# Kernel optimization log

Measured on AMD Instinct MI355X. Metric: run time of the kernel, lower is better.

## Reference

```python
import jax, jax.numpy as jnp
import numpy as np
from functools import partial

# --- constants from module init / yolov5 NMS conventions ---
CONF_THRES = 0.25
IOU_THRES = 0.45
PATCH_CONF = 0.001
GN = jnp.array([640.0, 640.0, 640.0, 640.0])  # img_size[[1,0,1,0]]
MAX_WH = 4096.0       # per-class NMS offset trick
K_CLEAN = 256         # fixed-size cap for clean detections (max_det=1000 effectively)
K_PATCH = 1024        # fixed-size cap for patch detections (max_det=30000 effectively)
MAXDET_CLEAN = 1000
MAXDET_PATCH = 30000
B, N, NC = 8, 25200, 80


def xywh2xyxy(x):
    xy, wh = x[..., :2], x[..., 2:4]
    return jnp.concatenate([xy - wh * 0.5, xy + wh * 0.5], axis=-1)


def pairwise_iou(a, b):
    # a: [A,4], b: [B,4] -> [A,B] jaccard overlap (same math as IoU.get_iou)
    tl = jnp.maximum(a[:, None, :2], b[None, :, :2])
    br = jnp.minimum(a[:, None, 2:], b[None, :, 2:])
    wh = jnp.clip(br - tl, 0.0)
    inter = wh[..., 0] * wh[..., 1]
    area_a = (a[:, 2] - a[:, 0]) * (a[:, 3] - a[:, 1])
    area_b = (b[:, 2] - b[:, 0]) * (b[:, 3] - b[:, 1])
    return inter / (area_a[:, None] + area_b[None, :] - inter)


def greedy_nms(iou_mat, valid, iou_thres):
    # iou_mat: [K,K] (score-sorted order), valid: [K] bool. Greedy suppression.
    K = valid.shape[0]
    j = jnp.arange(K)

    def body(i, keep):
        suppress = keep[i] & (iou_mat[i] > iou_thres) & (j > i)
        return keep & ~suppress

    return jax.lax.fori_loop(0, K, body, valid)


def _nms_single(pred, conf_thres, K, max_det):
    # pred: [N, 5+nc] raw yolov5 prediction for one image
    boxes = xywh2xyxy(pred[:, :4])
    obj = pred[:, 4]
    cls_scores = pred[:, 5:] * obj[:, None]          # conf = obj * cls
    conf = cls_scores.max(axis=-1)
    cls = jnp.argmax(cls_scores, axis=-1).astype(pred.dtype)
    valid = (obj > conf_thres) & (conf > conf_thres)
    mscore = jnp.where(valid, conf, -1.0)
    _, idx = jax.lax.top_k(mscore, K)                # fixed-size candidate prefilter
    bk, ck, vk = boxes[idx], cls[idx], valid[idx]
    off_boxes = bk + (ck * MAX_WH)[:, None]          # class-offset NMS
    iou = pairwise_iou(off_boxes, off_boxes)
    keep = greedy_nms(jax.lax.stop_gradient(iou), vk, IOU_THRES)
    keep = keep & (jnp.cumsum(keep.astype(jnp.int32)) <= max_det)
    return bk, ck, keep


def _forward(output_clean, output_patch):
    nms_clean = jax.vmap(lambda p: _nms_single(p, CONF_THRES, K_CLEAN, MAXDET_CLEAN))
    nms_patch = jax.vmap(lambda p: _nms_single(p, PATCH_CONF, K_PATCH, MAXDET_PATCH))
    bc, cc, kc = nms_clean(output_clean)   # [B,Kc,4],[B,Kc],[B,Kc]
    bp, cp, kp = nms_patch(output_patch)   # [B,Kp,4],[B,Kp],[B,Kp]
    bc_n = bc / GN
    bp_n = bp / GN

    def per_img(bp_i, cp_i, kp_i, bc_i, cc_i, kc_i):
        iou = pairwise_iou(bp_i, bc_i)                       # [Kp, Kc]
        match = kp_i[:, None] & (cp_i[:, None] == cc_i[None, :])
        tm = jnp.max(jnp.where(match, iou, 0.0), axis=0)     # max IoU per clean det
        return jnp.sum(jnp.where(kc_i, tm, 0.0)), jnp.sum(kc_i.astype(jnp.float32))

    sums, counts = jax.vmap(per_img)(bp_n, cp, kp, bc_n, cc, kc)
    total, cnt = sums.sum(), counts.sum()
    return jnp.where(cnt > 0, 1.0 - total / jnp.maximum(cnt, 1.0), 1.0)


def setup_inputs() -> dict:
    key = jax.random.key(0)
    k1, k2 = jax.random.split(key)

    def make(k):
        kxy, kwh, ko, kc = jax.random.split(k, 4)
        xy = jax.random.uniform(kxy, (B, N, 2)) * 608.0 + 16.0   # centers in-frame
        wh = jax.random.uniform(kwh, (B, N, 2)) * 96.0 + 8.0     # plausible box sizes
        obj = jax.random.uniform(ko, (B, N, 1))
        cls = jax.random.uniform(kc, (B, N, NC))
        return jnp.concatenate([xy, wh, obj, cls], axis=-1)

    return {"output_clean": make(k1), "output_patch": make(k2)}


def reference(output_clean, output_patch):
    return _forward(output_clean, output_patch)
```

## Files before the change

### kernel.cpp

```cpp
#include <hip/hip_runtime.h>

#define N_ANCH 25200
#define NCLS   80
#define ROW    85
#define NIMG   16
#define KMAX   1024
#define NBINS  4096
#define CAND_CAP 4096
#define SC_ROWS 64
#define SC_CHUNKS 394
#define SC_FLOATS (SC_ROWS*ROW)
#define PCHUNK 64
#define CCNT_STRIDE 16

typedef unsigned long long u64;
typedef unsigned int u32;

#define OFF_KEYS 0ull
#define OFF_HIST 3225600ull
#define OFF_TBIN 3487744ull
#define OFF_CCNT 3487808ull
#define OFF_SUMS 3488832ull
#define OFF_CNTS 3488864ull
#define OFF_CAND 3488896ull
#define OFF_SEL  4013184ull
#define OFF_BOX  4144256ull
#define OFF_CLS  4406400ull
#define OFF_RINIT 4471936ull
#define OFF_KEEP 4473984ull
#define WS_NEED  4539520ull
#define ZERO_BYTES (262144ull + 64 + 1024 + 32 + 32)

#define DMA16(gsrc, ldst) \
    __builtin_amdgcn_global_load_lds( \
        (const __attribute__((address_space(1))) void*)(gsrc), \
        (__attribute__((address_space(3))) void*)(ldst), 16, 0, 0)

__device__ __forceinline__ int key_bin(u64 key) {
    u32 hi = (u32)(key >> 32);
    if (hi == 0u) return 0;
    float conf = __uint_as_float(hi - 0x40000000u);
    int b = 1 + (int)(conf * 4093.0f);
    return b > 4094 ? 4094 : b;
}

__device__ __forceinline__ u64 readlane64(u64 v, int src) {
    u32 lo = (u32)__builtin_amdgcn_readlane((int)(u32)(v & 0xffffffffull), src);
    u32 hi = (u32)__builtin_amdgcn_readlane((int)(u32)(v >> 32), src);
    return ((u64)hi << 32) | (u64)lo;
}

__device__ __forceinline__ u64 shfl64_xor(u64 v, int m) {
    int lo = __shfl_xor((int)(u32)(v & 0xffffffffull), m, 64);
    int hi = __shfl_xor((int)(u32)(v >> 32), m, 64);
    return ((u64)(u32)hi << 32) | (u64)(u32)lo;
}

__global__ __launch_bounds__(128) void k_score(const float* __restrict__ clean,
                                               const float* __restrict__ patch,
                                               u64* __restrict__ keys)
{
    __shared__ float lbuf[SC_FLOATS];
    const int t = threadIdx.x;
    const int wv = t >> 6, lane = t & 63;
    const int bid = blockIdx.x;
    const int b = bid / SC_CHUNKS;
    const int chunk = bid - b * SC_CHUNKS;
    const float* bufbase = (b < 8) ? clean : patch;
    const float* ibase = bufbase + (size_t)((b < 8) ? b : b - 8) * N_ANCH * ROW;
    const int base = chunk * SC_ROWS;
    const float* g = ibase + (size_t)base * ROW;
    if (chunk != SC_CHUNKS - 1) {
        if (wv == 0) {
            #pragma unroll
            for (int u = 0; u < 11; ++u)
                DMA16(g + u * 256 + lane * 4, lbuf + u * 256);
        } else {
            #pragma unroll
            for (int u = 11; u < 21; ++u)
                DMA16(g + u * 256 + lane * 4, lbuf + u * 256);
            if (lane < 16)
                DMA16(g + 21 * 256 + lane * 4, lbuf + 21 * 256);
        }
    } else {
        const float* lim = bufbase + (size_t)8 * N_ANCH * ROW - 4;
        if (wv == 0) {
            #pragma unroll
            for (int u = 0; u < 11; ++u) {
                const float* s = g + u * 256 + lane * 4;
                if (s > lim) s = lim;
                DMA16(s, lbuf + u * 256);
            }
        } else {
            #pragma unroll
            for (int u = 11; u < 21; ++u) {
                const float* s = g + u * 256 + lane * 4;
                if (s > lim) s = lim;
                DMA16(s, lbuf + u * 256);
            }
            if (lane < 16) {
                const float* s = g + 21 * 256 + lane * 4;
                if (s > lim) s = lim;
                DMA16(s, lbuf + 21 * 256);
            }
        }
    }
    asm volatile("s_waitcnt vmcnt(0)" ::: "memory");
    __syncthreads();
    const int r = t >> 1, h = t & 1;
    const float* p = lbuf + r * ROW;
    const float obj = p[4];
    const int d0 = h * 40;
    float best = -1.0f; int bc = 0;
    #pragma unroll 8
    for (int d = 0; d < 40; ++d) {
        const float s = p[5 + d0 + d] * obj;
        if (s > best) { best = s; bc = d0 + d; }
    }
    const float obest = __shfl_xor(best, 1, 64);
    const int   obc   = __shfl_xor(bc, 1, 64);
    if (h == 0) {
        float fb = best; int fc = bc;
        if (obest > fb) { fb = obest; fc = obc; }
        const int row = base + r;
        if (row < N_ANCH) {
            const float th = (b < 8) ? 0.25f : 0.001f;
            const bool valid = (obj > th) && (fb > th);
            const u32 hi = valid ? (__float_as_uint(fb) + 0x40000000u) : 0u;
            const u32 nbar = 32767u - (u32)row;
            keys[(size_t)b * N_ANCH + row] =
                ((u64)hi << 32) | ((u64)nbar << 8) | (u64)(u32)fc;
        }
    }
}

__global__ __launch_bounds__(256) void k_hist(const u64* __restrict__ keys,
                                              int* __restrict__ hist)
{
    __shared__ int h[NBINS];
    const int b = blockIdx.x;
    for (int i = threadIdx.x; i < NBINS; i += 256) h[i] = 0;
    __syncthreads();
    const int start = blockIdx.y * 1575;
    const u64* kp = keys + (size_t)b * N_ANCH;
    for (int i = start + threadIdx.x; i < start + 1575; i += 256)
        atomicAdd(&h[key_bin(kp[i])], 1);
    __syncthreads();
    for (int i = threadIdx.x; i < NBINS; i += 256)
        if (h[i]) atomicAdd(&hist[b * NBINS + i], h[i]);
}

__global__ __launch_bounds__(1024) void k_thresh(const int* __restrict__ hist,
                                                 int* __restrict__ tbin)
{
    __shared__ int arr[1024];
    const int b = blockIdx.x;
    const int t = threadIdx.x;
    int hh[4];
    hh[0] = hist[b * NBINS + 4 * t + 0];
    hh[1] = hist[b * NBINS + 4 * t + 1];
    hh[2] = hist[b * NBINS + 4 * t + 2];
    hh[3] = hist[b * NBINS + 4 * t + 3];
    const int r = hh[0] + hh[1] + hh[2] + hh[3];
    arr[t] = r;
    __syncthreads();
    for (int off = 1; off < 1024; off <<= 1) {
        int v = (t + off < 1024) ? arr[t + off] : 0;
        __syncthreads();
        arr[t] += v;
        __syncthreads();
    }
    const int K = (b < 8) ? 256 : 1024;
    int cb = arr[t] - r;
    for (int d = 3; d >= 0; --d) {
        int ca = cb + hh[d];
        if (cb < K && ca >= K) tbin[b] = 4 * t + d;
        cb = ca;
    }
}

__global__ __launch_bounds__(256) void k_compact(const u64* __restrict__ keys,
                                                 const int* __restrict__ tbin,
                                                 int* __restrict__ ccnt,
                                                 u64* __restrict__ cand)
{
    const int b = blockIdx.x;
    const int T = tbin[b];
    const u64* kp = keys + (size_t)b * N_ANCH;
    const int start = blockIdx.y * 1575;
    const int lane = threadIdx.x & 63;
    #pragma unroll
    for (int it = 0; it < 7; ++it) {
        const int off = it * 256 + threadIdx.x;
        const bool in = off < 1575;
        const u64 key = in ? kp[start + off] : 0ull;
        const bool cnd = in && (key_bin(key) >= T);
        const u64 bal = __ballot(cnd);
        if (bal) {
            int base = 0;
            if (lane == 0) base = atomicAdd(&ccnt[b * CCNT_STRIDE], __popcll(bal));
            base = __shfl(base, 0, 64);
            if (cnd) {
                const int pos = base + __popcll(bal & ((1ull << lane) - 1ull));
                if (pos < CAND_CAP) cand[(size_t)b * CAND_CAP + pos] = key;
            }
        }
    }
}

__global__ __launch_bounds__(1024) void k_sort(const u64* __restrict__ cand,
                                               const int* __restrict__ ccnt,
                                               u64* __restrict__ sel)
{
    __shared__ u64 sk[CAND_CAP];
    const int b = blockIdx.x;
    const int C = min(ccnt[b * CCNT_STRIDE], CAND_CAP);
    const int t = threadIdx.x;
    #pragma unroll
    for (int p = 0; p < CAND_CAP / 1024; ++p) {
        int i = p * 1024 + t;
        sk[i] = (i < C) ? cand[(size_t)b * CAND_CAP + i] : 0ull;
    }
    __syncthreads();
    for (int k = 2; k <= CAND_CAP; k <<= 1) {
        for (int j = k >> 1; j > 0; j >>= 1) {
            #pragma unroll
            for (int p = 0; p < CAND_CAP / 1024; ++p) {
                int i = p * 1024 + t;
                int ixj = i ^ j;
                if (ixj > i) {
                    u64 a = sk[i], c = sk[ixj];
                    bool descSeg = ((i & k) == 0);
                    bool sw = descSeg ? (a < c) : (a > c);
                    if (sw) { sk[i] = c; sk[ixj] = a; }
                }
            }
            __syncthreads();
        }
    }
    const int K = (b < 8) ? 256 : 1024;
    if (t < K) sel[b * KMAX + t] = sk[t];
}

__global__ __launch_bounds__(1024) void k_gather(const float* __restrict__ clean,
                                                 const float* __restrict__ patch,
                                                 const u64* __restrict__ sel,
                                                 float4* __restrict__ boxes,
                                                 int* __restrict__ cls,
                                                 u64* __restrict__ rinit)
{
    const int b = blockIdx.x;
    const int t = threadIdx.x;
    const int K = (b < 8) ? 256 : 1024;
    const u64 key = (t < K) ? sel[b * KMAX + t] : 0ull;
    const u32 hi = (u32)(key >> 32);
    const bool valid = (t < K) && (hi != 0u);
    u64 bal = __ballot(valid);
    if ((t & 63) == 0) rinit[b * 16 + (t >> 6)] = ~bal;
    if (t >= K) return;
    const int n = 32767 - (int)((key >> 8) & 0x7FFFu);
    const int c = (int)(key & 0x7Fu);
    const float* src = ((b < 8) ? (clean + (size_t)b * N_ANCH * ROW)
                                : (patch + (size_t)(b - 8) * N_ANCH * ROW)) + (size_t)n * ROW;
    const float x = src[0], y = src[1], w = src[2], h = src[3];
    boxes[b * KMAX + t] = make_float4(x - w * 0.5f, y - h * 0.5f, x + w * 0.5f, y + h * 0.5f);
    cls[b * KMAX + t] = c;
}

__global__ __launch_bounds__(1024) void k_nms_mask(const float4* __restrict__ boxes,
                                                   const int* __restrict__ cls,
                                                   u64* __restrict__ mask,
                                                   u64* __restrict__ diag)
{
    __shared__ float4 bx[KMAX];
    __shared__ float ar[KMAX];
    const int b = blockIdx.x;
    const int K = (b < 8) ? 256 : 1024;
    const int row0 = blockIdx.y * 64;
    if (row0 >= K) return;
    const int t = threadIdx.x;
    for (int i = t; i < K; i += 1024) {
        float4 v = boxes[b * KMAX + i];
        float off = (float)cls[b * KMAX + i] * 4096.0f;
        v.x += off; v.y += off; v.z += off; v.w += off;
        bx[i] = v;
        ar[i] = (v.z - v.x) * (v.w - v.y);
    }
    __syncthreads();
    const int w   = t >> 6;
    const int row = row0 + (t & 63);
    u64* dst = mask + ((size_t)b * KMAX + row) * 16 + w;
    if (((w << 6) + 63) <= row0 && row0 > 0) { *dst = 0ull; return; }
    const float4 bi = bx[row];
    const float ai = ar[row];
    const int jbase = w << 6;
    u64 m = 0;
    #pragma unroll 8
    for (int k = 0; k < 64; ++k) {
        const int j = jbase + k;
        const float4 bj = bx[j];
        const float ax = fmaxf(bi.x, bj.x), ay = fmaxf(bi.y, bj.y);
        const float bx2 = fminf(bi.z, bj.z), by2 = fminf(bi.w, bj.w);
        const float iw = fmaxf(bx2 - ax, 0.f), ih = fmaxf(by2 - ay, 0.f);
        const float inter = iw * ih;
        const float iou = inter / (ai + ar[j] - inter);
        if (j > row && iou > 0.45f) m |= (1ull << k);
    }
    *dst = m;
    if (w == (row0 >> 6)) diag[(size_t)b * KMAX + row] = m;
}

__global__ __launch_bounds__(1024) void k_nms_scan(const u64* __restrict__ mask,
                                                   const u64* __restrict__ diag,
                                                   const u64* __restrict__ rinit,
                                                   int* __restrict__ keep)
{
    extern __shared__ u64 smem[];
    const int b = blockIdx.x;
    const int K = (b < 8) ? 256 : 1024;
    const int W = K >> 6;
    const int t = threadIdx.x;
    u64* smask = smem;
    u64* sdiag = smem + (size_t)K * 16;
    {
        const float4* s4 = (const float4*)(mask + (size_t)b * KMAX * 16);
        float4* d4 = (float4*)smask;
        const int n4 = (K * 16) >> 1;
        for (int i = t; i < n4; i += 1024) d4[i] = s4[i];
        const float4* s4d = (const float4*)(diag + (size_t)b * KMAX);
        float4* d4d = (float4*)sdiag;
        for (int i = t; i < (K >> 1); i += 1024) d4d[i] = s4d[i];
    }
    __syncthreads();
    if (t >= 64) return;
    const int lane = t;
    const int q = lane >> 4;
    const int wl = lane & 15;
    u64 w_remv = rinit[b * 16 + wl];
    u64 ow = readlane64(w_remv, 0);
    u64 dj = sdiag[lane];
    for (int g = 0; g < W; ++g) {
        u64 nz = __ballot(dj != 0ull);
        u64 o = ow;
        while (nz) {
            const int j = (int)__builtin_ctzll(nz);
            nz &= nz - 1;
            if (!((o >> j) & 1ull)) o |= readlane64(dj, j);
        }
        const u64 kept = ~o;
        if (g + 1 < W) dj = sdiag[(g + 1) * 64 + lane];
        const u64* mrow = smask + (size_t)(g * 64 + q * 16) * 16 + wl;
        const u32 kg = (u32)((kept >> (q * 16)) & 0xFFFFull);
        u64 a0 = 0, a1 = 0;
        #pragma unroll
        for (int i = 0; i < 16; i += 2) {
            const u64 m0 = mrow[(size_t)(i + 0) * 16];
            const u64 m1 = mrow[(size_t)(i + 1) * 16];
            a0 |= ((kg >> i) & 1u) ? m0 : 0ull;
            a1 |= ((kg >> (i + 1)) & 1u) ? m1 : 0ull;
        }
        u64 part = a0 | a1;
        part |= shfl64_xor(part, 16);
        part |= shfl64_xor(part, 32);
        w_remv |= part;
        if (g + 1 < W) ow = readlane64(w_remv, g + 1);
    }
    if (lane < W) {
        #pragma unroll
        for (int k = 0; k < 64; ++k)
            keep[b * KMAX + lane * 64 + k] = (int)(((w_remv >> k) & 1) ^ 1ull);
    }
}

__global__ __launch_bounds__(256) void k_match_partial(const float4* __restrict__ boxes,
                                                       const int* __restrict__ cls,
                                                       const int* __restrict__ keep,
                                                       float* __restrict__ pmax)
{
    __shared__ float4 pb[PCHUNK];
    __shared__ float par[PCHUNK];
    __shared__ int pcls[PCHUNK];
    const int c = blockIdx.x;
    const int p = blockIdx.y;
    const int bp = 8 + c;
    const int t = threadIdx.x;
    if (t < PCHUNK) {
        const int i = p * PCHUNK + t;
        const float4 v = boxes[bp * KMAX + i];
        pb[t] = v;
        par[t] = (v.z - v.x) * (v.w - v.y);
        pcls[t] = keep[bp * KMAX + i] ? cls[bp * KMAX + i] : -1;
    }
    __syncthreads();
    const float4 bc = boxes[c * KMAX + t];
    const int cc = cls[c * KMAX + t];
    const float area_c = (bc.z - bc.x) * (bc.w - bc.y);
    float tm = 0.f;
    #pragma unroll 8
    for (int i = 0; i < PCHUNK; ++i) {
        const float4 bi = pb[i];
        const float ax = fmaxf(bi.x, bc.x), ay = fmaxf(bi.y, bc.y);
        const float bx2 = fminf(bi.z, bc.z), by2 = fminf(bi.w, bc.w);
        const float iw = fmaxf(bx2 - ax, 0.f), ih = fmaxf(by2 - ay, 0.f);
        const float inter = iw * ih;
        const float iou = inter / (par[i] + area_c - inter);
        tm = fmaxf(tm, (pcls[i] == cc) ? iou : 0.f);
    }
    pmax[(c * 16 + p) * 256 + t] = tm;
}

__global__ __launch_bounds__(256) void k_match_reduce(const float* __restrict__ pmax,
                                                      const int* __restrict__ keep,
                                                      float* __restrict__ sums,
                                                      float* __restrict__ cnts)
{
    __shared__ float red[8];
    const int c = blockIdx.x;
    const int t = threadIdx.x;
    float tm = 0.f;
    #pragma unroll
    for (int p = 0; p < 16; ++p)
        tm = fmaxf(tm, pmax[(c * 16 + p) * 256 + t]);
    const int kc = keep[c * KMAX + t];
    float val = kc ? tm : 0.f;
    float cv  = kc ? 1.f : 0.f;
    for (int off = 32; off > 0; off >>= 1) {
        val += __shfl_down(val, off);
        cv  += __shfl_down(cv, off);
    }
    const int wv = t >> 6, lane = t & 63;
    if (lane == 0) { red[wv] = val; red[4 + wv] = cv; }
    __syncthreads();
    if (t == 0) {
        sums[c] = red[0] + red[1] + red[2] + red[3];
        cnts[c] = red[4] + red[5] + red[6] + red[7];
    }
}

__global__ void k_final(const float* __restrict__ sums,
                        const float* __restrict__ cnts,
                        float* __restrict__ out)
{
    if (threadIdx.x == 0 && blockIdx.x == 0) {
        float total = 0.f, cnt = 0.f;
        for (int c = 0; c < 8; ++c) { total += sums[c]; cnt += cnts[c]; }
        out[0] = (cnt > 0.f) ? (1.0f - total / fmaxf(cnt, 1.0f)) : 1.0f;
    }
}

extern "C" void kernel_launch(void* const* d_in, const int* in_sizes, int n_in,
                              void* d_out, int out_size, void* d_ws, size_t ws_size,
                              hipStream_t stream)
{
    if (ws_size < WS_NEED) return;
    const float* clean = (const float*)d_in[0];
    const float* patch = (const float*)d_in[1];
    float* out = (float*)d_out;
    char* ws = (char*)d_ws;

    u64*    keys = (u64*)(ws + OFF_KEYS);
    u64*    mask = (u64*)(ws + OFF_KEYS);
    int*    hist = (int*)(ws + OFF_HIST);
    u64*    diag = (u64*)(ws + OFF_HIST);
    int*    tbin = (int*)(ws + OFF_TBIN);
    int*    ccnt = (int*)(ws + OFF_CCNT);
    float*  sums = (float*)(ws + OFF_SUMS);
    float*  cnts = (float*)(ws + OFF_CNTS);
    u64*    cand = (u64*)(ws + OFF_CAND);
    float*  pmax = (float*)(ws + OFF_CAND);
    u64*    sel  = (u64*)(ws + OFF_SEL);
    float4* boxes = (float4*)(ws + OFF_BOX);
    int*    cls  = (int*)(ws + OFF_CLS);
    u64*    rinit = (u64*)(ws + OFF_RINIT);
    int*    keep = (int*)(ws + OFF_KEEP);

    hipMemsetAsync(ws + OFF_HIST, 0, ZERO_BYTES, stream);

    k_score<<<NIMG * SC_CHUNKS, 128, 0, stream>>>(clean, patch, keys);
    k_hist<<<dim3(NIMG, 16), 256, 0, stream>>>(keys, hist);
    k_thresh<<<NIMG, 1024, 0, stream>>>(hist, tbin);
    k_compact<<<dim3(NIMG, 16), 256, 0, stream>>>(keys, tbin, ccnt, cand);
    k_sort<<<NIMG, 1024, 0, stream>>>(cand, ccnt, sel);
    k_gather<<<NIMG, 1024, 0, stream>>>(clean, patch, sel, boxes, cls, rinit);
    k_nms_mask<<<dim3(NIMG, 16), 1024, 0, stream>>>(boxes, cls, mask, diag);
    k_nms_scan<<<NIMG, 1024, KMAX * 16 * 8 + KMAX * 8, stream>>>(mask, diag, rinit, keep);
    k_match_partial<<<dim3(8, 16), 256, 0, stream>>>(boxes, cls, keep, pmax);
    k_match_reduce<<<8, 256, 0, stream>>>(pmax, keep, sums, cnts);
    k_final<<<1, 64, 0, stream>>>(sums, cnts, out);
}
```

Before: 137.2 us.

## Double-buffer persistent score kernel and register-resident bitonic sort with shuffles

The score kernel becomes a persistent grid in which each wave streams 16-row chunks through double-buffered LDS, issuing the next chunk's async copies before computing the current one. This is meant to overlap global loads with compute and remove the block-wide barrier. The bitonic sort now keeps four elements per thread in registers, using in-register swaps for strides of 1024 and above, wave shuffles for strides below 64, and LDS only for the strides in between. That removes most LDS round trips and syncs, at the cost of more complex index logic and a tie-break rule changed to prefer the lower class.

```diff
diff --git a/kernel.cpp b/kernel.cpp
--- a/kernel.cpp
+++ b/kernel.cpp
@@ -7,9 +7,11 @@
 #define KMAX   1024
 #define NBINS  4096
 #define CAND_CAP 4096
-#define SC_ROWS 64
-#define SC_CHUNKS 394
-#define SC_FLOATS (SC_ROWS*ROW)
+#define SC2_RPC 16
+#define SC2_CPI 1575
+#define SC2_CHUNKS (NIMG * SC2_CPI)
+#define SC2_CFLOATS (SC2_RPC * ROW)
+#define SC2_BLOCKS 1792
 #define PCHUNK 64
 #define CCNT_STRIDE 16
 
@@ -56,81 +58,74 @@
     return ((u64)(u32)hi << 32) | (u64)(u32)lo;
 }
 
+__device__ __forceinline__ void sc_issue(const float* __restrict__ clean,
+                                         const float* __restrict__ patch,
+                                         int c, int lane, float* buf)
+{
+    const int b = c / SC2_CPI;
+    const int ch = c - b * SC2_CPI;
+    const float* g = ((b < 8) ? clean + (size_t)b * N_ANCH * ROW
+                              : patch + (size_t)(b - 8) * N_ANCH * ROW)
+                     + (size_t)ch * SC2_CFLOATS;
+    #pragma unroll
+    for (int u = 0; u < 5; ++u)
+        DMA16(g + u * 256 + lane * 4, buf + u * 256);
+    if (lane < 20)
+        DMA16(g + 5 * 256 + lane * 4, buf + 5 * 256);
+}
+
+__device__ __forceinline__ void sc_compute(int c, int lane,
+                                           const float* buf, u64* __restrict__ keys)
+{
+    const int b = c / SC2_CPI;
+    const int ch = c - b * SC2_CPI;
+    const int r = lane & 15, h = lane >> 4;
+    const float* p = buf + r * ROW;
+    const float obj = p[4];
+    float best = -1.0f; int bc = 0;
+    #pragma unroll
+    for (int d = 0; d < 20; ++d) {
+        const float s = p[5 + h * 20 + d] * obj;
+        if (s > best) { best = s; bc = h * 20 + d; }
+    }
+    #pragma unroll
+    for (int m = 16; m <= 32; m <<= 1) {
+        const float o = __shfl_xor(best, m, 64);
+        const int  oc = __shfl_xor(bc, m, 64);
+        if (o > best || (o == best && oc < bc)) { best = o; bc = oc; }
+    }
+    if (h == 0) {
+        const int n = ch * SC2_RPC + r;
+        const float th = (b < 8) ? 0.25f : 0.001f;
+        const bool valid = (obj > th) && (best > th);
+        const u32 hi = valid ? (__float_as_uint(best) + 0x40000000u) : 0u;
+        const u32 nbar = 32767u - (u32)n;
+        keys[(size_t)b * N_ANCH + n] =
+            ((u64)hi << 32) | ((u64)nbar << 8) | (u64)(u32)bc;
+    }
+}
+
 __global__ __launch_bounds__(128) void k_score(const float* __restrict__ clean,
                                                const float* __restrict__ patch,
                                                u64* __restrict__ keys)
 {
-    __shared__ float lbuf[SC_FLOATS];
-    const int t = threadIdx.x;
-    const int wv = t >> 6, lane = t & 63;
-    const int bid = blockIdx.x;
-    const int b = bid / SC_CHUNKS;
-    const int chunk = bid - b * SC_CHUNKS;
-    const float* bufbase = (b < 8) ? clean : patch;
-    const float* ibase = bufbase + (size_t)((b < 8) ? b : b - 8) * N_ANCH * ROW;
-    const int base = chunk * SC_ROWS;
-    const float* g = ibase + (size_t)base * ROW;
-    if (chunk != SC_CHUNKS - 1) {
-        if (wv == 0) {
-            #pragma unroll
-            for (int u = 0; u < 11; ++u)
-                DMA16(g + u * 256 + lane * 4, lbuf + u * 256);
+    __shared__ float lds[2][2][SC2_CFLOATS];
+    const int wv = threadIdx.x >> 6, lane = threadIdx.x & 63;
+    const int wid = blockIdx.x * 2 + wv;
+    const int stride = SC2_BLOCKS * 2;
+    int cur = 0;
+    sc_issue(clean, patch, wid, lane, &lds[wv][0][0]);
+    for (int c = wid; c < SC2_CHUNKS; c += stride) {
+        const int cn = c + stride;
+        if (cn < SC2_CHUNKS) {
+            sc_issue(clean, patch, cn, lane, &lds[wv][cur ^ 1][0]);
+            asm volatile("s_waitcnt vmcnt(6)" ::: "memory");
         } else {
-            #pragma unroll
-            for (int u = 11; u < 21; ++u)
-                DMA16(g + u * 256 + lane * 4, lbuf + u * 256);
-            if (lane < 16)
-                DMA16(g + 21 * 256 + lane * 4, lbuf + 21 * 256);
+            asm volatile("s_waitcnt vmcnt(0)" ::: "memory");
         }
-    } else {
-        const float* lim = bufbase + (size_t)8 * N_ANCH * ROW - 4;
-        if (wv == 0) {
-            #pragma unroll
-            for (int u = 0; u < 11; ++u) {
-                const float* s = g + u * 256 + lane * 4;
-                if (s > lim) s = lim;
-                DMA16(s, lbuf + u * 256);
-            }
-        } else {
-            #pragma unroll
-            for (int u = 11; u < 21; ++u) {
-                const float* s = g + u * 256 + lane * 4;
-                if (s > lim) s = lim;
-                DMA16(s, lbuf + u * 256);
-            }
-            if (lane < 16) {
-                const float* s = g + 21 * 256 + lane * 4;
-                if (s > lim) s = lim;
-                DMA16(s, lbuf + 21 * 256);
-            }
-        }
-    }
-    asm volatile("s_waitcnt vmcnt(0)" ::: "memory");
-    __syncthreads();
-    const int r = t >> 1, h = t & 1;
-    const float* p = lbuf + r * ROW;
-    const float obj = p[4];
-    const int d0 = h * 40;
-    float best = -1.0f; int bc = 0;
-    #pragma unroll 8
-    for (int d = 0; d < 40; ++d) {
-        const float s = p[5 + d0 + d] * obj;
-        if (s > best) { best = s; bc = d0 + d; }
-    }
-    const float obest = __shfl_xor(best, 1, 64);
-    const int   obc   = __shfl_xor(bc, 1, 64);
-    if (h == 0) {
-        float fb = best; int fc = bc;
-        if (obest > fb) { fb = obest; fc = obc; }
-        const int row = base + r;
-        if (row < N_ANCH) {
-            const float th = (b < 8) ? 0.25f : 0.001f;
-            const bool valid = (obj > th) && (fb > th);
-            const u32 hi = valid ? (__float_as_uint(fb) + 0x40000000u) : 0u;
-            const u32 nbar = 32767u - (u32)row;
-            keys[(size_t)b * N_ANCH + row] =
-                ((u64)hi << 32) | ((u64)nbar << 8) | (u64)(u32)fc;
-        }
+        __builtin_amdgcn_sched_barrier(0);
+        sc_compute(c, lane, &lds[wv][cur][0], keys);
+        cur ^= 1;
     }
 }
 
@@ -216,30 +211,61 @@
     const int b = blockIdx.x;
     const int C = min(ccnt[b * CCNT_STRIDE], CAND_CAP);
     const int t = threadIdx.x;
-    #pragma unroll
-    for (int p = 0; p < CAND_CAP / 1024; ++p) {
-        int i = p * 1024 + t;
-        sk[i] = (i < C) ? cand[(size_t)b * CAND_CAP + i] : 0ull;
-    }
-    __syncthreads();
-    for (int k = 2; k <= CAND_CAP; k <<= 1) {
+    u64 e0, e1, e2, e3;
+    e0 = (t < C) ? cand[(size_t)b * CAND_CAP + t] : 0ull;
+    e1 = (1024 + t < C) ? cand[(size_t)b * CAND_CAP + 1024 + t] : 0ull;
+    e2 = (2048 + t < C) ? cand[(size_t)b * CAND_CAP + 2048 + t] : 0ull;
+    e3 = (3072 + t < C) ? cand[(size_t)b * CAND_CAP + 3072 + t] : 0ull;
+
+    #define CSWAP_D(a, c) { if ((a) < (c)) { u64 _t = (a); (a) = (c); (c) = _t; } }
+    #define CSWAP_A(a, c) { if ((a) > (c)) { u64 _t = (a); (a) = (c); (c) = _t; } }
+
+    for (int k = 2; k <= 4096; k <<= 1) {
         for (int j = k >> 1; j > 0; j >>= 1) {
-            #pragma unroll
-            for (int p = 0; p < CAND_CAP / 1024; ++p) {
-                int i = p * 1024 + t;
-                int ixj = i ^ j;
-                if (ixj > i) {
-                    u64 a = sk[i], c = sk[ixj];
-                    bool descSeg = ((i & k) == 0);
-                    bool sw = descSeg ? (a < c) : (a > c);
-                    if (sw) { sk[i] = c; sk[ixj] = a; }
+            if (j >= 1024) {
+                if (j == 2048) {
+                    CSWAP_D(e0, e2); CSWAP_D(e1, e3);
+                } else {
+                    if (k == 4096) { CSWAP_D(e0, e1); CSWAP_D(e2, e3); }
+                    else           { CSWAP_D(e0, e1); CSWAP_A(e2, e3); }
+                }
+            } else if (j >= 64) {
+                __syncthreads();
+                sk[t] = e0; sk[1024 + t] = e1; sk[2048 + t] = e2; sk[3072 + t] = e3;
+                __syncthreads();
+                const int tp = t ^ j;
+                #pragma unroll
+                for (int p = 0; p < 4; ++p) {
+                    const int i = p * 1024 + t;
+                    const u64 cv = (p == 0) ? e0 : (p == 1) ? e1 : (p == 2) ? e2 : e3;
+                    const u64 o = sk[p * 1024 + tp];
+                    const bool take_max = (((i & k) == 0) == ((t & j) == 0));
+                    const u64 mx = cv > o ? cv : o;
+                    const u64 mn = cv > o ? o : cv;
+                    const u64 nv = take_max ? mx : mn;
+                    if (p == 0) e0 = nv; else if (p == 1) e1 = nv;
+                    else if (p == 2) e2 = nv; else e3 = nv;
+                }
+            } else {
+                #pragma unroll
+                for (int p = 0; p < 4; ++p) {
+                    const int i = p * 1024 + t;
+                    const u64 cv = (p == 0) ? e0 : (p == 1) ? e1 : (p == 2) ? e2 : e3;
+                    const u64 o = shfl64_xor(cv, j);
+                    const bool take_max = (((i & k) == 0) == ((t & j) == 0));
+                    const u64 mx = cv > o ? cv : o;
+                    const u64 mn = cv > o ? o : cv;
+                    const u64 nv = take_max ? mx : mn;
+                    if (p == 0) e0 = nv; else if (p == 1) e1 = nv;
+                    else if (p == 2) e2 = nv; else e3 = nv;
                 }
             }
-            __syncthreads();
         }
     }
     const int K = (b < 8) ? 256 : 1024;
-    if (t < K) sel[b * KMAX + t] = sk[t];
+    if (t < K) sel[b * KMAX + t] = e0;
+    #undef CSWAP_D
+    #undef CSWAP_A
 }
 
 __global__ __launch_bounds__(1024) void k_gather(const float* __restrict__ clean,
@@ -476,7 +502,7 @@
 
     hipMemsetAsync(ws + OFF_HIST, 0, ZERO_BYTES, stream);
 
-    k_score<<<NIMG * SC_CHUNKS, 128, 0, stream>>>(clean, patch, keys);
+    k_score<<<SC2_BLOCKS, 128, 0, stream>>>(clean, patch, keys);
     k_hist<<<dim3(NIMG, 16), 256, 0, stream>>>(keys, hist);
     k_thresh<<<NIMG, 1024, 0, stream>>>(hist, tbin);
     k_compact<<<dim3(NIMG, 16), 256, 0, stream>>>(keys, tbin, ccnt, cand);
```

After: 136.1 us. Within noise of the previous version (-0.8%).
